# Performance work log

Measured on AMD Instinct MI355X. Metric: run time of the kernel, lower is better.

Reference implementation:

```python
import jax, jax.numpy as jnp
import numpy as np

N = 50000
E = 800000
IN, HID, OUT, HEADS = 128, 64, 64, 3
NEG_SLOPE = 0.2
BN_EPS = 1e-5


def setup_inputs() -> dict:
    key = jax.random.key(0)
    ks = jax.random.split(key, 20)
    s = 0.05
    inp = {
        "x": jax.random.normal(ks[0], (N, IN), jnp.float32),
        "edge_index": jax.random.randint(ks[1], (2, E), 0, N, jnp.int32),
        # layer 0: in=128 -> heads=3, C=64 (concat -> 192)
        "Wl0": jax.random.normal(ks[2], (IN, HEADS * HID), jnp.float32) * s,
        "bl0": jnp.zeros((HEADS * HID,), jnp.float32),
        "Wr0": jax.random.normal(ks[3], (IN, HEADS * HID), jnp.float32) * s,
        "br0": jnp.zeros((HEADS * HID,), jnp.float32),
        "att0": jax.random.normal(ks[4], (HEADS, HID), jnp.float32) * s,
        "bias0": jnp.zeros((HEADS * HID,), jnp.float32),
        "gamma0": jnp.ones((HEADS * HID,), jnp.float32),
        "beta0": jnp.zeros((HEADS * HID,), jnp.float32),
        # layer 1: in=192 -> heads=1, C=64
        "Wl1": jax.random.normal(ks[5], (HEADS * HID, OUT), jnp.float32) * s,
        "bl1": jnp.zeros((OUT,), jnp.float32),
        "Wr1": jax.random.normal(ks[6], (HEADS * HID, OUT), jnp.float32) * s,
        "br1": jnp.zeros((OUT,), jnp.float32),
        "att1": jax.random.normal(ks[7], (1, OUT), jnp.float32) * s,
        "bias1": jnp.zeros((OUT,), jnp.float32),
        "gamma1": jnp.ones((OUT,), jnp.float32),
        "beta1": jnp.zeros((OUT,), jnp.float32),
    }
    return inp


def _gatv2_layer(x, Wl, bl, Wr, br, att, bias, src, dst, n):
    H, C = att.shape
    xl = (x @ Wl + bl).reshape(n, H, C)
    xr = (x @ Wr + br).reshape(n, H, C)
    e = jax.nn.leaky_relu(xl[src] + xr[dst], NEG_SLOPE)      # [E,H,C]
    logit = jnp.einsum("ehc,hc->eh", e, att)                 # [E,H]
    m = jax.lax.stop_gradient(jax.ops.segment_max(logit, dst, num_segments=n))
    p = jnp.exp(logit - m[dst])
    denom = jax.ops.segment_sum(p, dst, num_segments=n)
    alpha = p / denom[dst]                                   # per-dst softmax
    out = jax.ops.segment_sum(alpha[:, :, None] * xl[src], dst, num_segments=n)
    return out.reshape(n, H * C) + bias


def _bn(x, gamma, beta):
    mu = x.mean(0)
    var = x.var(0)
    return (x - mu) * jax.lax.rsqrt(var + BN_EPS) * gamma + beta


def reference(x, edge_index, Wl0, bl0, Wr0, br0, att0, bias0, gamma0, beta0,
              Wl1, bl1, Wr1, br1, att1, bias1, gamma1, beta1):
    n = x.shape[0]
    loops = jnp.arange(n, dtype=edge_index.dtype)
    src = jnp.concatenate([edge_index[0], loops])  # PyG add_self_loops=True
    dst = jnp.concatenate([edge_index[1], loops])
    h = _gatv2_layer(x, Wl0, bl0, Wr0, br0, att0, bias0, src, dst, n)
    h = _bn(jax.nn.relu(h), gamma0, beta0)
    h = _gatv2_layer(h, Wl1, bl1, Wr1, br1, att1, bias1, src, dst, n)
    h = _bn(jax.nn.relu(h), gamma1, beta1)
    return h
```

## Files before the change

kernel.cpp:

```cpp
#include <hip/hip_runtime.h>
#include <hip/hip_bf16.h>

#define LRELU_SLOPE 0.2f
#define BN_EPS 1e-5f

typedef __attribute__((ext_vector_type(8))) short short8v;
typedef __attribute__((ext_vector_type(4))) float float4v;

static __device__ __forceinline__ unsigned short f2bf(float f) {
    __hip_bfloat16 b = __float2bfloat16(f);
    return *reinterpret_cast<unsigned short*>(&b);
}
static __device__ __forceinline__ float bf2f(unsigned short u) {
    return __uint_as_float(((unsigned)u) << 16);
}
static __device__ __forceinline__ void unpack2(unsigned int u, float& f0, float& f1) {
    f0 = __uint_as_float(u << 16);
    f1 = __uint_as_float(u & 0xffff0000u);
}

__global__ void convert_w2_kernel(const float* __restrict__ Wl0, const float* __restrict__ Wr0,
                                  const float* __restrict__ Wl1, const float* __restrict__ Wr1,
                                  unsigned short* __restrict__ Wt0, unsigned short* __restrict__ Wt1) {
    int idx = blockIdx.x * blockDim.x + threadIdx.x;
    if (idx < 384 * 128) {
        int c = idx >> 7, k = idx & 127;
        float v = (c < 192) ? Wl0[(size_t)k * 192 + c] : Wr0[(size_t)k * 192 + (c - 192)];
        Wt0[idx] = f2bf(v);
    } else if (idx < 384 * 128 + 128 * 192) {
        int i2 = idx - 384 * 128;
        int c = i2 / 192, k = i2 % 192;
        float v = (c < 64) ? Wl1[(size_t)k * 64 + c] : Wr1[(size_t)k * 64 + (c - 64)];
        Wt1[i2] = f2bf(v);
    }
}

__global__ void count_dst_kernel(const int* __restrict__ dst, int* __restrict__ counts, int E) {
    int e = blockIdx.x * blockDim.x + threadIdx.x;
    if (e < E) atomicAdd(&counts[dst[e]], 1);
}

__global__ void scanA_kernel(const int* __restrict__ counts, int* __restrict__ offs,
                             int* __restrict__ blkSum, int n) {
    __shared__ int wsum[4];
    const int lane = threadIdx.x & 63;
    const int wv = threadIdx.x >> 6;
    int i0 = blockIdx.x * 1024 + (int)threadIdx.x * 4;
    int v0 = (i0 + 0 < n) ? counts[i0 + 0] : 0;
    int v1 = (i0 + 1 < n) ? counts[i0 + 1] : 0;
    int v2 = (i0 + 2 < n) ? counts[i0 + 2] : 0;
    int v3 = (i0 + 3 < n) ? counts[i0 + 3] : 0;
    int s4 = v0 + v1 + v2 + v3;
    int s = s4;
    #pragma unroll
    for (int off = 1; off < 64; off <<= 1) {
        int t = __shfl_up(s, off, 64);
        if (lane >= off) s += t;
    }
    if (lane == 63) wsum[wv] = s;
    __syncthreads();
    int wpre = 0;
    for (int w = 0; w < wv; ++w) wpre += wsum[w];
    int excl = wpre + s - s4;
    if (i0 + 0 < n) offs[i0 + 0] = excl;
    excl += v0;
    if (i0 + 1 < n) offs[i0 + 1] = excl;
    excl += v1;
    if (i0 + 2 < n) offs[i0 + 2] = excl;
    excl += v2;
    if (i0 + 3 < n) offs[i0 + 3] = excl;
    if (threadIdx.x == 255) blkSum[blockIdx.x] = wpre + s;
}

__global__ void scanC_kernel(int* __restrict__ offs, const int* __restrict__ blkSum, int n, int E) {
    __shared__ int baseSh;
    const int b = blockIdx.x;
    if (threadIdx.x < 64) {
        int acc = 0;
        for (int i = threadIdx.x; i < b; i += 64) acc += blkSum[i];
        #pragma unroll
        for (int off = 1; off < 64; off <<= 1) acc += __shfl_xor(acc, off, 64);
        if (threadIdx.x == 0) baseSh = acc;
    }
    __syncthreads();
    const int base = baseSh;
    int i = b * 1024 + (int)threadIdx.x * 4;
    if (i + 3 < n) {
        int4 v = *reinterpret_cast<int4*>(&offs[i]);
        v.x += base; v.y += base; v.z += base; v.w += base;
        *reinterpret_cast<int4*>(&offs[i]) = v;
    } else {
        #pragma unroll
        for (int k = 0; k < 4; ++k)
            if (i + k < n) offs[i + k] += base;
    }
    if (b == 0 && threadIdx.x == 0) offs[n] = E;
}

__global__ void scatter_kernel(const int* __restrict__ src, const int* __restrict__ dst,
                               const int* __restrict__ offs, int* __restrict__ cursor,
                               int* __restrict__ esrc, int E) {
    int e = blockIdx.x * blockDim.x + threadIdx.x;
    if (e < E) {
        int d = dst[e];
        int pos = offs[d] + atomicAdd(&cursor[d], 1);
        esrc[pos] = src[e];
    }
}

template <int K, int NCH, bool BN>
__global__ __launch_bounds__(256) void mfma_dual_gemm(
    const float* __restrict__ X,
    const unsigned short* __restrict__ Wt,
    const float* __restrict__ bl, const float* __restrict__ br,
    const float* __restrict__ stats, const float* __restrict__ gamma,
    const float* __restrict__ beta, float invN,
    unsigned short* __restrict__ out, int N) {
    constexpr int ST = 2 * NCH;
    constexpr int LDA = 40;
    const int rowBase = blockIdx.x * 128;
    const int colBase = blockIdx.y * 128;

    __shared__ unsigned short XS[128 * LDA];
    __shared__ unsigned short WS[128 * LDA];
    __shared__ float ssA[K], ssB[K];

    const int tid = threadIdx.x;
    const int lane = tid & 63;
    const int wv = tid >> 6;
    const int lrow = lane & 15;
    const int lk = lane >> 4;

    if (BN) {
        for (int c = tid; c < K; c += 256) {
            float mu = stats[c] * invN;
            float var = stats[K + c] * invN - mu * mu;
            float sc = gamma[c] * rsqrtf(var + BN_EPS);
            ssA[c] = sc;
            ssB[c] = beta[c] - mu * sc;
        }
        __syncthreads();
    }

    float4v acc[2][8];
    #pragma unroll
    for (int i = 0; i < 2; ++i)
        #pragma unroll
        for (int j = 0; j < 8; ++j) acc[i][j] = (float4v){0.f, 0.f, 0.f, 0.f};

    for (int k0 = 0; k0 < K; k0 += 32) {
        {
            int r = tid >> 3;
            int kq = (tid & 7) * 4;
            float4 sc0, sc1;
            if (BN) {
                sc0 = *reinterpret_cast<const float4*>(&ssA[k0 + kq]);
                sc1 = *reinterpret_cast<const float4*>(&ssB[k0 + kq]);
            }
            #pragma unroll
            for (int i = 0; i < 4; ++i) {
                int row = r + 32 * i;
                int gr = rowBase + row;
                float4 v = make_float4(0.f, 0.f, 0.f, 0.f);
                if (gr < N) v = *reinterpret_cast<const float4*>(&X[(size_t)gr * K + k0 + kq]);
                if (BN) {
                    v.x = v.x * sc0.x + sc1.x;
                    v.y = v.y * sc0.y + sc1.y;
                    v.z = v.z * sc0.z + sc1.z;
                    v.w = v.w * sc0.w + sc1.w;
                }
                ushort4 u;
                u.x = f2bf(v.x); u.y = f2bf(v.y); u.z = f2bf(v.z); u.w = f2bf(v.w);
                *reinterpret_cast<ushort4*>(&XS[row * LDA + kq]) = u;
            }
        }
        {
            int c = tid >> 2;
            int kq8 = (tid & 3) * 8;
            #pragma unroll
            for (int i = 0; i < 2; ++i) {
                int col = c + 64 * i;
                uint4 w = *reinterpret_cast<const uint4*>(&Wt[(size_t)(colBase + col) * K + k0 + kq8]);
                *reinterpret_cast<uint4*>(&WS[col * LDA + kq8]) = w;
            }
        }
        __syncthreads();
        short8v aF[2], bF[8];
        #pragma unroll
        for (int rb = 0; rb < 2; ++rb)
            aF[rb] = *reinterpret_cast<const short8v*>(&XS[(wv * 32 + rb * 16 + lrow) * LDA + lk * 8]);
        #pragma unroll
        for (int cb = 0; cb < 8; ++cb)
            bF[cb] = *reinterpret_cast<const short8v*>(&WS[(cb * 16 + lrow) * LDA + lk * 8]);
        #pragma unroll
        for (int rb = 0; rb < 2; ++rb)
            #pragma unroll
            for (int cb = 0; cb < 8; ++cb)
                acc[rb][cb] = __builtin_amdgcn_mfma_f32_16x16x32_bf16(aF[rb], bF[cb], acc[rb][cb], 0, 0, 0);
        __syncthreads();
    }
    #pragma unroll
    for (int cb = 0; cb < 8; ++cb) {
        int cg = colBase + cb * 16 + lrow;
        float bv = (cg < NCH) ? bl[cg] : br[cg - NCH];
        #pragma unroll
        for (int rb = 0; rb < 2; ++rb) {
            #pragma unroll
            for (int r = 0; r < 4; ++r) {
                int row = rowBase + wv * 32 + rb * 16 + lk * 4 + r;
                if (row < N) out[(size_t)row * ST + cg] = f2bf(acc[rb][cb][r] + bv);
            }
        }
    }
}

template <int H>
__global__ __launch_bounds__(256) void gat_agg_kernel(
    const unsigned short* __restrict__ proj,
    const int* __restrict__ offs, const int* __restrict__ esrc,
    const float* __restrict__ att, const float* __restrict__ bias,
    float* __restrict__ outh, int N) {
    constexpr int C = 64;
    constexpr int HC = H * C;
    constexpr int ST = 2 * HC;
    const int lane = threadIdx.x & 63;
    const int node = blockIdx.x * 4 + (threadIdx.x >> 6);
    if (node >= N) return;
    const int j = lane >> 4;
    const int cg = (lane & 15) * 4;

    float4 xr4[H], att4[H], acc4[H];
    float den[H];
    #pragma unroll
    for (int h = 0; h < H; ++h) {
        ushort4 u = *reinterpret_cast<const ushort4*>(&proj[(size_t)node * ST + HC + h * C + cg]);
        xr4[h] = make_float4(bf2f(u.x), bf2f(u.y), bf2f(u.z), bf2f(u.w));
        att4[h] = *reinterpret_cast<const float4*>(&att[h * C + cg]);
        acc4[h] = make_float4(0.f, 0.f, 0.f, 0.f);
        den[h] = 0.f;
    }

    const int beg = offs[node];
    const int total = offs[node + 1] - beg + 1;
    int vc0 = (j < total) ? j : (total - 1);
    int srcN = (vc0 == 0) ? node : esrc[beg + vc0 - 1];
    ushort4 uN[H];
    #pragma unroll
    for (int h = 0; h < H; ++h)
        uN[h] = *reinterpret_cast<const ushort4*>(&proj[(size_t)srcN * ST + h * C + cg]);

    for (int t = 0; t < total; t += 4) {
        ushort4 uC[H];
        #pragma unroll
        for (int h = 0; h < H; ++h) uC[h] = uN[h];
        const int v = t + j;
        const float w = (v < total) ? 1.f : 0.f;
        const int v2 = v + 4;
        if (v2 < total) {
            int s2 = esrc[beg + v2 - 1];
            #pragma unroll
            for (int h = 0; h < H; ++h)
                uN[h] = *reinterpret_cast<const ushort4*>(&proj[(size_t)s2 * ST + h * C + cg]);
        }
        float4 xl4[H];
        float s[H];
        #pragma unroll
        for (int h = 0; h < H; ++h)
            xl4[h] = make_float4(bf2f(uC[h].x), bf2f(uC[h].y), bf2f(uC[h].z), bf2f(uC[h].w));
        #pragma unroll
        for (int h = 0; h < H; ++h) {
            float a0 = xl4[h].x + xr4[h].x;
            float a1 = xl4[h].y + xr4[h].y;
            float a2 = xl4[h].z + xr4[h].z;
            float a3 = xl4[h].w + xr4[h].w;
            a0 = (a0 > 0.f) ? a0 : LRELU_SLOPE * a0;
            a1 = (a1 > 0.f) ? a1 : LRELU_SLOPE * a1;
            a2 = (a2 > 0.f) ? a2 : LRELU_SLOPE * a2;
            a3 = (a3 > 0.f) ? a3 : LRELU_SLOPE * a3;
            s[h] = a0 * att4[h].x + a1 * att4[h].y + a2 * att4[h].z + a3 * att4[h].w;
        }
        #pragma unroll
        for (int off = 1; off <= 8; off <<= 1)
            #pragma unroll
            for (int h = 0; h < H; ++h) s[h] += __shfl_xor(s[h], off, 64);
        #pragma unroll
        for (int h = 0; h < H; ++h) {
            float p = w * __expf(s[h]);
            den[h] += p;
            acc4[h].x += p * xl4[h].x;
            acc4[h].y += p * xl4[h].y;
            acc4[h].z += p * xl4[h].z;
            acc4[h].w += p * xl4[h].w;
        }
    }

    #pragma unroll
    for (int off = 16; off <= 32; off <<= 1) {
        #pragma unroll
        for (int h = 0; h < H; ++h) {
            acc4[h].x += __shfl_xor(acc4[h].x, off, 64);
            acc4[h].y += __shfl_xor(acc4[h].y, off, 64);
            acc4[h].z += __shfl_xor(acc4[h].z, off, 64);
            acc4[h].w += __shfl_xor(acc4[h].w, off, 64);
            den[h]    += __shfl_xor(den[h],    off, 64);
        }
    }

    if (j == 0) {
        #pragma unroll
        for (int h = 0; h < H; ++h) {
            float4 b4 = *reinterpret_cast<const float4*>(&bias[h * C + cg]);
            float inv = 1.f / den[h];
            float4 o;
            o.x = acc4[h].x * inv + b4.x;
            o.y = acc4[h].y * inv + b4.y;
            o.z = acc4[h].z * inv + b4.z;
            o.w = acc4[h].w * inv + b4.w;
            o.x = (o.x > 0.f) ? o.x : 0.f;
            o.y = (o.y > 0.f) ? o.y : 0.f;
            o.z = (o.z > 0.f) ? o.z : 0.f;
            o.w = (o.w > 0.f) ? o.w : 0.f;
            *reinterpret_cast<float4*>(&outh[(size_t)node * HC + h * C + cg]) = o;
        }
    }
}

__global__ __launch_bounds__(256) void gat_agg1_kernel(
    const unsigned short* __restrict__ proj,
    const int* __restrict__ offs, const int* __restrict__ esrc,
    const float* __restrict__ att, const float* __restrict__ bias,
    float* __restrict__ outh, int N) {
    const int lane = threadIdx.x & 63;
    const int node = blockIdx.x * 4 + (threadIdx.x >> 6);
    if (node >= N) return;
    const int j = lane >> 3;
    const int cg = (lane & 7) * 8;

    float xr[8], at[8], acc[8];
    float den = 0.f;
    {
        uint4 u = *reinterpret_cast<const uint4*>(&proj[(size_t)node * 128 + 64 + cg]);
        unpack2(u.x, xr[0], xr[1]); unpack2(u.y, xr[2], xr[3]);
        unpack2(u.z, xr[4], xr[5]); unpack2(u.w, xr[6], xr[7]);
        float4 a0 = *reinterpret_cast<const float4*>(&att[cg]);
        float4 a1 = *reinterpret_cast<const float4*>(&att[cg + 4]);
        at[0] = a0.x; at[1] = a0.y; at[2] = a0.z; at[3] = a0.w;
        at[4] = a1.x; at[5] = a1.y; at[6] = a1.z; at[7] = a1.w;
        #pragma unroll
        for (int c = 0; c < 8; ++c) acc[c] = 0.f;
    }

    const int beg = offs[node];
    const int total = offs[node + 1] - beg + 1;
    int vc0 = (j < total) ? j : (total - 1);
    int srcN = (vc0 == 0) ? node : esrc[beg + vc0 - 1];
    uint4 uN = *reinterpret_cast<const uint4*>(&proj[(size_t)srcN * 128 + cg]);

    for (int t = 0; t < total; t += 8) {
        uint4 uC = uN;
        const int v = t + j;
        const float w = (v < total) ? 1.f : 0.f;
        const int v2 = v + 8;
        if (v2 < total) {
            int s2 = esrc[beg + v2 - 1];
            uN = *reinterpret_cast<const uint4*>(&proj[(size_t)s2 * 128 + cg]);
        }
        float xl[8];
        unpack2(uC.x, xl[0], xl[1]); unpack2(uC.y, xl[2], xl[3]);
        unpack2(uC.z, xl[4], xl[5]); unpack2(uC.w, xl[6], xl[7]);
        float s = 0.f;
        #pragma unroll
        for (int c = 0; c < 8; ++c) {
            float a = xl[c] + xr[c];
            a = (a > 0.f) ? a : LRELU_SLOPE * a;
            s += a * at[c];
        }
        #pragma unroll
        for (int off = 1; off <= 4; off <<= 1) s += __shfl_xor(s, off, 64);
        float p = w * __expf(s);
        den += p;
        #pragma unroll
        for (int c = 0; c < 8; ++c) acc[c] += p * xl[c];
    }

    #pragma unroll
    for (int off = 8; off <= 32; off <<= 1) {
        den += __shfl_xor(den, off, 64);
        #pragma unroll
        for (int c = 0; c < 8; ++c) acc[c] += __shfl_xor(acc[c], off, 64);
    }

    if (j == 0) {
        float inv = 1.f / den;
        float4 b0 = *reinterpret_cast<const float4*>(&bias[cg]);
        float4 b1 = *reinterpret_cast<const float4*>(&bias[cg + 4]);
        float4 o0, o1;
        o0.x = acc[0] * inv + b0.x; o0.y = acc[1] * inv + b0.y;
        o0.z = acc[2] * inv + b0.z; o0.w = acc[3] * inv + b0.w;
        o1.x = acc[4] * inv + b1.x; o1.y = acc[5] * inv + b1.y;
        o1.z = acc[6] * inv + b1.z; o1.w = acc[7] * inv + b1.w;
        o0.x = (o0.x > 0.f) ? o0.x : 0.f; o0.y = (o0.y > 0.f) ? o0.y : 0.f;
        o0.z = (o0.z > 0.f) ? o0.z : 0.f; o0.w = (o0.w > 0.f) ? o0.w : 0.f;
        o1.x = (o1.x > 0.f) ? o1.x : 0.f; o1.y = (o1.y > 0.f) ? o1.y : 0.f;
        o1.z = (o1.z > 0.f) ? o1.z : 0.f; o1.w = (o1.w > 0.f) ? o1.w : 0.f;
        *reinterpret_cast<float4*>(&outh[(size_t)node * 64 + cg]) = o0;
        *reinterpret_cast<float4*>(&outh[(size_t)node * 64 + cg + 4]) = o1;
    }
}

template <int CH>
__global__ void bn_stats_kernel(const float* __restrict__ h, float* __restrict__ stats, int N) {
    const int c = threadIdx.x;
    float s = 0.f, q = 0.f;
    for (int r = blockIdx.x; r < N; r += gridDim.x) {
        float v = h[(size_t)r * CH + c];
        s += v;
        q += v * v;
    }
    atomicAdd(&stats[c], s);
    atomicAdd(&stats[CH + c], q);
}

__global__ void bn_finapply64_kernel(float* __restrict__ h, const float* __restrict__ stats,
                                     const float* __restrict__ gamma, const float* __restrict__ beta,
                                     float invN, size_t total4) {
    size_t i = (size_t)blockIdx.x * blockDim.x + threadIdx.x;
    if (i >= total4) return;
    size_t e = i * 4;
    int c = (int)(e & 63);
    float4 v = *reinterpret_cast<float4*>(&h[e]);
    #pragma unroll
    for (int k = 0; k < 4; ++k) {
        float mu = stats[c + k] * invN;
        float var = stats[64 + c + k] * invN - mu * mu;
        float sc = gamma[c + k] * rsqrtf(var + BN_EPS);
        (&v.x)[k] = ((&v.x)[k] - mu) * sc + beta[c + k];
    }
    *reinterpret_cast<float4*>(&h[e]) = v;
}

extern "C" void kernel_launch(void* const* d_in, const int* in_sizes, int n_in,
                              void* d_out, int out_size, void* d_ws, size_t ws_size,
                              hipStream_t stream) {
    const float* x     = (const float*)d_in[0];
    const int*   eidx  = (const int*)d_in[1];
    const float* Wl0   = (const float*)d_in[2];
    const float* bl0   = (const float*)d_in[3];
    const float* Wr0   = (const float*)d_in[4];
    const float* br0   = (const float*)d_in[5];
    const float* att0  = (const float*)d_in[6];
    const float* bias0 = (const float*)d_in[7];
    const float* g0    = (const float*)d_in[8];
    const float* be0   = (const float*)d_in[9];
    const float* Wl1   = (const float*)d_in[10];
    const float* bl1   = (const float*)d_in[11];
    const float* Wr1   = (const float*)d_in[12];
    const float* br1   = (const float*)d_in[13];
    const float* att1  = (const float*)d_in[14];
    const float* bias1 = (const float*)d_in[15];
    const float* g1    = (const float*)d_in[16];
    const float* be1   = (const float*)d_in[17];

    const int N = in_sizes[0] / 128;
    const int E = in_sizes[1] / 2;
    const int* srcIdx = eidx;
    const int* dstIdx = eidx + E;
    const int nChunks = (N + 1023) >> 10;
    const float invN = 1.f / (float)N;

    char* base = (char*)d_ws;
    auto alloc = [&](size_t bytes) {
        char* p = base;
        base += (bytes + 255) & ~(size_t)255;
        return p;
    };
    unsigned short* proj = (unsigned short*)alloc((size_t)N * 384 * 2);
    float* h0    = (float*)alloc((size_t)N * 192 * 4);
    int*   offs  = (int*)alloc((size_t)(N + 1) * 4);
    int*   esrc  = (int*)alloc((size_t)E * 4);
    int*   blkSum= (int*)alloc((size_t)nChunks * 4);
    unsigned short* Wt0 = (unsigned short*)alloc((size_t)384 * 128 * 2);
    unsigned short* Wt1 = (unsigned short*)alloc((size_t)128 * 192 * 2);
    char* zeroBeg = base;
    int*   counts = (int*)alloc((size_t)N * 4);
    int*   cursor = (int*)alloc((size_t)N * 4);
    float* stats0 = (float*)alloc(384 * 4);
    float* stats1 = (float*)alloc(128 * 4);
    size_t zeroBytes = (size_t)(base - zeroBeg);

    hipMemsetAsync(zeroBeg, 0, zeroBytes, stream);
    convert_w2_kernel<<<(384 * 128 + 128 * 192 + 255) / 256, 256, 0, stream>>>(Wl0, Wr0, Wl1, Wr1, Wt0, Wt1);

    count_dst_kernel<<<(E + 255) / 256, 256, 0, stream>>>(dstIdx, counts, E);
    scanA_kernel<<<nChunks, 256, 0, stream>>>(counts, offs, blkSum, N);
    scanC_kernel<<<nChunks, 256, 0, stream>>>(offs, blkSum, N, E);
    scatter_kernel<<<(E + 255) / 256, 256, 0, stream>>>(srcIdx, dstIdx, offs, cursor, esrc, E);

    {
        dim3 grid((N + 127) / 128, 3);
        mfma_dual_gemm<128, 192, false><<<grid, 256, 0, stream>>>(
            x, Wt0, bl0, br0, nullptr, nullptr, nullptr, 0.f, proj, N);
    }
    gat_agg_kernel<3><<<(N + 3) / 4, 256, 0, stream>>>(proj, offs, esrc, att0, bias0, h0, N);
    bn_stats_kernel<192><<<256, 192, 0, stream>>>(h0, stats0, N);

    {
        dim3 grid((N + 127) / 128, 1);
        mfma_dual_gemm<192, 64, true><<<grid, 256, 0, stream>>>(
            h0, Wt1, bl1, br1, stats0, g0, be0, invN, proj, N);
    }
    float* out = (float*)d_out;
    gat_agg1_kernel<<<(N + 3) / 4, 256, 0, stream>>>(proj, offs, esrc, att1, bias1, out, N);
    bn_stats_kernel<64><<<256, 64, 0, stream>>>(out, stats1, N);
    {
        size_t tot4 = (size_t)N * 16;
        bn_finapply64_kernel<<<(unsigned)((tot4 + 255) / 256), 256, 0, stream>>>(out, stats1, g1, be1, invN, tot4);
    }
}
```

Measured before the change: 378.3 us.

## Fuse BN statistics into GAT aggregation with persistent blocks and deeper prefetch

The separate bn_stats kernels are removed. Each aggregation kernel now accumulates per-channel sum and sum-of-squares in LDS atomics and flushes them to global memory once per block. The kernels become grid-stride persistent with at most 1536 blocks, and the neighbor gather prefetch is deepened from one iteration ahead to two. This avoids re-reading h0 and the output for statistics, at the cost of LDS atomic contention and fewer resident blocks.

```diff
diff --git a/kernel.cpp b/kernel.cpp
--- a/kernel.cpp
+++ b/kernel.cpp
@@ -17,6 +17,9 @@
 static __device__ __forceinline__ void unpack2(unsigned int u, float& f0, float& f1) {
     f0 = __uint_as_float(u << 16);
     f1 = __uint_as_float(u & 0xffff0000u);
+}
+static __device__ __forceinline__ float lrelu(float x) {
+    return fmaxf(x, LRELU_SLOPE * x);
 }
 
 __global__ void convert_w2_kernel(const float* __restrict__ Wl0, const float* __restrict__ Wr0,
@@ -214,211 +217,227 @@
     }
 }
 
-template <int H>
-__global__ __launch_bounds__(256) void gat_agg_kernel(
+__global__ __launch_bounds__(256) void gat_agg3_bn_kernel(
     const unsigned short* __restrict__ proj,
     const int* __restrict__ offs, const int* __restrict__ esrc,
     const float* __restrict__ att, const float* __restrict__ bias,
-    float* __restrict__ outh, int N) {
-    constexpr int C = 64;
-    constexpr int HC = H * C;
-    constexpr int ST = 2 * HC;
-    const int lane = threadIdx.x & 63;
-    const int node = blockIdx.x * 4 + (threadIdx.x >> 6);
-    if (node >= N) return;
+    float* __restrict__ outh, float* __restrict__ stats,
+    int N, int nGroups) {
+    constexpr int H = 3, C = 64, HC = 192, ST = 384;
+    __shared__ float ldsStats[2 * HC];
+    const int tid = threadIdx.x;
+    const int lane = tid & 63;
+    const int wv = tid >> 6;
     const int j = lane >> 4;
     const int cg = (lane & 15) * 4;
 
-    float4 xr4[H], att4[H], acc4[H];
-    float den[H];
+    for (int i = tid; i < 2 * HC; i += 256) ldsStats[i] = 0.f;
+    __syncthreads();
+
+    float4 att4[H];
     #pragma unroll
-    for (int h = 0; h < H; ++h) {
-        ushort4 u = *reinterpret_cast<const ushort4*>(&proj[(size_t)node * ST + HC + h * C + cg]);
-        xr4[h] = make_float4(bf2f(u.x), bf2f(u.y), bf2f(u.z), bf2f(u.w));
-        att4[h] = *reinterpret_cast<const float4*>(&att[h * C + cg]);
-        acc4[h] = make_float4(0.f, 0.f, 0.f, 0.f);
-        den[h] = 0.f;
-    }
-
-    const int beg = offs[node];
-    const int total = offs[node + 1] - beg + 1;
-    int vc0 = (j < total) ? j : (total - 1);
-    int srcN = (vc0 == 0) ? node : esrc[beg + vc0 - 1];
-    ushort4 uN[H];
-    #pragma unroll
-    for (int h = 0; h < H; ++h)
-        uN[h] = *reinterpret_cast<const ushort4*>(&proj[(size_t)srcN * ST + h * C + cg]);
-
-    for (int t = 0; t < total; t += 4) {
-        ushort4 uC[H];
-        #pragma unroll
-        for (int h = 0; h < H; ++h) uC[h] = uN[h];
-        const int v = t + j;
-        const float w = (v < total) ? 1.f : 0.f;
-        const int v2 = v + 4;
-        if (v2 < total) {
-            int s2 = esrc[beg + v2 - 1];
+    for (int h = 0; h < H; ++h) att4[h] = *reinterpret_cast<const float4*>(&att[h * C + cg]);
+
+    for (int g = blockIdx.x; g < nGroups; g += gridDim.x) {
+        const int node = g * 4 + wv;
+        if (node >= N) continue;
+        float4 xr4[H], acc4[H];
+        float den[H];
+        #pragma unroll
+        for (int h = 0; h < H; ++h) {
+            ushort4 u = *reinterpret_cast<const ushort4*>(&proj[(size_t)node * ST + HC + h * C + cg]);
+            xr4[h] = make_float4(bf2f(u.x), bf2f(u.y), bf2f(u.z), bf2f(u.w));
+            acc4[h] = make_float4(0.f, 0.f, 0.f, 0.f);
+            den[h] = 0.f;
+        }
+        const int beg = offs[node];
+        const int total = offs[node + 1] - beg + 1;
+        ushort4 u0[H], u1[H];
+        {
+            int vc = (j < total) ? j : (total - 1);
+            int s0 = (vc == 0) ? node : esrc[beg + vc - 1];
             #pragma unroll
             for (int h = 0; h < H; ++h)
-                uN[h] = *reinterpret_cast<const ushort4*>(&proj[(size_t)s2 * ST + h * C + cg]);
-        }
-        float4 xl4[H];
-        float s[H];
-        #pragma unroll
-        for (int h = 0; h < H; ++h)
-            xl4[h] = make_float4(bf2f(uC[h].x), bf2f(uC[h].y), bf2f(uC[h].z), bf2f(uC[h].w));
-        #pragma unroll
-        for (int h = 0; h < H; ++h) {
-            float a0 = xl4[h].x + xr4[h].x;
-            float a1 = xl4[h].y + xr4[h].y;
-            float a2 = xl4[h].z + xr4[h].z;
-            float a3 = xl4[h].w + xr4[h].w;
-            a0 = (a0 > 0.f) ? a0 : LRELU_SLOPE * a0;
-            a1 = (a1 > 0.f) ? a1 : LRELU_SLOPE * a1;
-            a2 = (a2 > 0.f) ? a2 : LRELU_SLOPE * a2;
-            a3 = (a3 > 0.f) ? a3 : LRELU_SLOPE * a3;
-            s[h] = a0 * att4[h].x + a1 * att4[h].y + a2 * att4[h].z + a3 * att4[h].w;
-        }
-        #pragma unroll
-        for (int off = 1; off <= 8; off <<= 1)
-            #pragma unroll
-            for (int h = 0; h < H; ++h) s[h] += __shfl_xor(s[h], off, 64);
-        #pragma unroll
-        for (int h = 0; h < H; ++h) {
-            float p = w * __expf(s[h]);
-            den[h] += p;
-            acc4[h].x += p * xl4[h].x;
-            acc4[h].y += p * xl4[h].y;
-            acc4[h].z += p * xl4[h].z;
-            acc4[h].w += p * xl4[h].w;
-        }
-    }
-
-    #pragma unroll
-    for (int off = 16; off <= 32; off <<= 1) {
-        #pragma unroll
-        for (int h = 0; h < H; ++h) {
-            acc4[h].x += __shfl_xor(acc4[h].x, off, 64);
-            acc4[h].y += __shfl_xor(acc4[h].y, off, 64);
-            acc4[h].z += __shfl_xor(acc4[h].z, off, 64);
-            acc4[h].w += __shfl_xor(acc4[h].w, off, 64);
-            den[h]    += __shfl_xor(den[h],    off, 64);
-        }
-    }
-
-    if (j == 0) {
-        #pragma unroll
-        for (int h = 0; h < H; ++h) {
-            float4 b4 = *reinterpret_cast<const float4*>(&bias[h * C + cg]);
-            float inv = 1.f / den[h];
-            float4 o;
-            o.x = acc4[h].x * inv + b4.x;
-            o.y = acc4[h].y * inv + b4.y;
-            o.z = acc4[h].z * inv + b4.z;
-            o.w = acc4[h].w * inv + b4.w;
-            o.x = (o.x > 0.f) ? o.x : 0.f;
-            o.y = (o.y > 0.f) ? o.y : 0.f;
-            o.z = (o.z > 0.f) ? o.z : 0.f;
-            o.w = (o.w > 0.f) ? o.w : 0.f;
-            *reinterpret_cast<float4*>(&outh[(size_t)node * HC + h * C + cg]) = o;
-        }
-    }
-}
-
-__global__ __launch_bounds__(256) void gat_agg1_kernel(
+                u0[h] = *reinterpret_cast<const ushort4*>(&proj[(size_t)s0 * ST + h * C + cg]);
+            int v1i = j + 4;
+            int vc1 = (v1i < total) ? v1i : (total - 1);
+            int s1 = (vc1 == 0) ? node : esrc[beg + vc1 - 1];
+            #pragma unroll
+            for (int h = 0; h < H; ++h)
+                u1[h] = *reinterpret_cast<const ushort4*>(&proj[(size_t)s1 * ST + h * C + cg]);
+        }
+        for (int t = 0; t < total; t += 4) {
+            float4 xl4[H];
+            #pragma unroll
+            for (int h = 0; h < H; ++h) {
+                xl4[h] = make_float4(bf2f(u0[h].x), bf2f(u0[h].y), bf2f(u0[h].z), bf2f(u0[h].w));
+                u0[h] = u1[h];
+            }
+            const int v2 = t + 8 + j;
+            if (v2 < total) {
+                int s2 = esrc[beg + v2 - 1];
+                #pragma unroll
+                for (int h = 0; h < H; ++h)
+                    u1[h] = *reinterpret_cast<const ushort4*>(&proj[(size_t)s2 * ST + h * C + cg]);
+            }
+            float s[H];
+            #pragma unroll
+            for (int h = 0; h < H; ++h) {
+                float a0 = lrelu(xl4[h].x + xr4[h].x);
+                float a1 = lrelu(xl4[h].y + xr4[h].y);
+                float a2 = lrelu(xl4[h].z + xr4[h].z);
+                float a3 = lrelu(xl4[h].w + xr4[h].w);
+                s[h] = a0 * att4[h].x + a1 * att4[h].y + a2 * att4[h].z + a3 * att4[h].w;
+            }
+            #pragma unroll
+            for (int off = 1; off <= 8; off <<= 1)
+                #pragma unroll
+                for (int h = 0; h < H; ++h) s[h] += __shfl_xor(s[h], off, 64);
+            const float w = (t + j < total) ? 1.f : 0.f;
+            #pragma unroll
+            for (int h = 0; h < H; ++h) {
+                float p = w * __expf(s[h]);
+                den[h] += p;
+                acc4[h].x += p * xl4[h].x;
+                acc4[h].y += p * xl4[h].y;
+                acc4[h].z += p * xl4[h].z;
+                acc4[h].w += p * xl4[h].w;
+            }
+        }
+        #pragma unroll
+        for (int off = 16; off <= 32; off <<= 1) {
+            #pragma unroll
+            for (int h = 0; h < H; ++h) {
+                acc4[h].x += __shfl_xor(acc4[h].x, off, 64);
+                acc4[h].y += __shfl_xor(acc4[h].y, off, 64);
+                acc4[h].z += __shfl_xor(acc4[h].z, off, 64);
+                acc4[h].w += __shfl_xor(acc4[h].w, off, 64);
+                den[h]    += __shfl_xor(den[h],    off, 64);
+            }
+        }
+        if (j == 0) {
+            #pragma unroll
+            for (int h = 0; h < H; ++h) {
+                float4 b4 = *reinterpret_cast<const float4*>(&bias[h * C + cg]);
+                float inv = 1.f / den[h];
+                float4 o;
+                o.x = fmaxf(acc4[h].x * inv + b4.x, 0.f);
+                o.y = fmaxf(acc4[h].y * inv + b4.y, 0.f);
+                o.z = fmaxf(acc4[h].z * inv + b4.z, 0.f);
+                o.w = fmaxf(acc4[h].w * inv + b4.w, 0.f);
+                *reinterpret_cast<float4*>(&outh[(size_t)node * HC + h * C + cg]) = o;
+                atomicAdd(&ldsStats[h * C + cg + 0], o.x);
+                atomicAdd(&ldsStats[h * C + cg + 1], o.y);
+                atomicAdd(&ldsStats[h * C + cg + 2], o.z);
+                atomicAdd(&ldsStats[h * C + cg + 3], o.w);
+                atomicAdd(&ldsStats[HC + h * C + cg + 0], o.x * o.x);
+                atomicAdd(&ldsStats[HC + h * C + cg + 1], o.y * o.y);
+                atomicAdd(&ldsStats[HC + h * C + cg + 2], o.z * o.z);
+                atomicAdd(&ldsStats[HC + h * C + cg + 3], o.w * o.w);
+            }
+        }
+    }
+    __syncthreads();
+    for (int i = tid; i < 2 * HC; i += 256) atomicAdd(&stats[i], ldsStats[i]);
+}
+
+__global__ __launch_bounds__(256) void gat_agg1_bn_kernel(
     const unsigned short* __restrict__ proj,
     const int* __restrict__ offs, const int* __restrict__ esrc,
     const float* __restrict__ att, const float* __restrict__ bias,
-    float* __restrict__ outh, int N) {
-    const int lane = threadIdx.x & 63;
-    const int node = blockIdx.x * 4 + (threadIdx.x >> 6);
-    if (node >= N) return;
+    float* __restrict__ outh, float* __restrict__ stats,
+    int N, int nGroups) {
+    __shared__ float ldsStats[128];
+    const int tid = threadIdx.x;
+    const int lane = tid & 63;
+    const int wv = tid >> 6;
     const int j = lane >> 3;
     const int cg = (lane & 7) * 8;
 
-    float xr[8], at[8], acc[8];
-    float den = 0.f;
+    for (int i = tid; i < 128; i += 256) ldsStats[i] = 0.f;
+    __syncthreads();
+
+    float at[8];
     {
-        uint4 u = *reinterpret_cast<const uint4*>(&proj[(size_t)node * 128 + 64 + cg]);
-        unpack2(u.x, xr[0], xr[1]); unpack2(u.y, xr[2], xr[3]);
-        unpack2(u.z, xr[4], xr[5]); unpack2(u.w, xr[6], xr[7]);
         float4 a0 = *reinterpret_cast<const float4*>(&att[cg]);
         float4 a1 = *reinterpret_cast<const float4*>(&att[cg + 4]);
         at[0] = a0.x; at[1] = a0.y; at[2] = a0.z; at[3] = a0.w;
         at[4] = a1.x; at[5] = a1.y; at[6] = a1.z; at[7] = a1.w;
-        #pragma unroll
-        for (int c = 0; c < 8; ++c) acc[c] = 0.f;
-    }
-
-    const int beg = offs[node];
-    const int total = offs[node + 1] - beg + 1;
-    int vc0 = (j < total) ? j : (total - 1);
-    int srcN = (vc0 == 0) ? node : esrc[beg + vc0 - 1];
-    uint4 uN = *reinterpret_cast<const uint4*>(&proj[(size_t)srcN * 128 + cg]);
-
-    for (int t = 0; t < total; t += 8) {
-        uint4 uC = uN;
-        const int v = t + j;
-        const float w = (v < total) ? 1.f : 0.f;
-        const int v2 = v + 8;
-        if (v2 < total) {
-            int s2 = esrc[beg + v2 - 1];
-            uN = *reinterpret_cast<const uint4*>(&proj[(size_t)s2 * 128 + cg]);
-        }
-        float xl[8];
-        unpack2(uC.x, xl[0], xl[1]); unpack2(uC.y, xl[2], xl[3]);
-        unpack2(uC.z, xl[4], xl[5]); unpack2(uC.w, xl[6], xl[7]);
-        float s = 0.f;
-        #pragma unroll
-        for (int c = 0; c < 8; ++c) {
-            float a = xl[c] + xr[c];
-            a = (a > 0.f) ? a : LRELU_SLOPE * a;
-            s += a * at[c];
-        }
-        #pragma unroll
-        for (int off = 1; off <= 4; off <<= 1) s += __shfl_xor(s, off, 64);
-        float p = w * __expf(s);
-        den += p;
-        #pragma unroll
-        for (int c = 0; c < 8; ++c) acc[c] += p * xl[c];
-    }
-
-    #pragma unroll
-    for (int off = 8; off <= 32; off <<= 1) {
-        den += __shfl_xor(den, off, 64);
-        #pragma unroll
-        for (int c = 0; c < 8; ++c) acc[c] += __shfl_xor(acc[c], off, 64);
-    }
-
-    if (j == 0) {
-        float inv = 1.f / den;
-        float4 b0 = *reinterpret_cast<const float4*>(&bias[cg]);
-        float4 b1 = *reinterpret_cast<const float4*>(&bias[cg + 4]);
-        float4 o0, o1;
-        o0.x = acc[0] * inv + b0.x; o0.y = acc[1] * inv + b0.y;
-        o0.z = acc[2] * inv + b0.z; o0.w = acc[3] * inv + b0.w;
-        o1.x = acc[4] * inv + b1.x; o1.y = acc[5] * inv + b1.y;
-        o1.z = acc[6] * inv + b1.z; o1.w = acc[7] * inv + b1.w;
-        o0.x = (o0.x > 0.f) ? o0.x : 0.f; o0.y = (o0.y > 0.f) ? o0.y : 0.f;
-        o0.z = (o0.z > 0.f) ? o0.z : 0.f; o0.w = (o0.w > 0.f) ? o0.w : 0.f;
-        o1.x = (o1.x > 0.f) ? o1.x : 0.f; o1.y = (o1.y > 0.f) ? o1.y : 0.f;
-        o1.z = (o1.z > 0.f) ? o1.z : 0.f; o1.w = (o1.w > 0.f) ? o1.w : 0.f;
-        *reinterpret_cast<float4*>(&outh[(size_t)node * 64 + cg]) = o0;
-        *reinterpret_cast<float4*>(&outh[(size_t)node * 64 + cg + 4]) = o1;
-    }
-}
-
-template <int CH>
-__global__ void bn_stats_kernel(const float* __restrict__ h, float* __restrict__ stats, int N) {
-    const int c = threadIdx.x;
-    float s = 0.f, q = 0.f;
-    for (int r = blockIdx.x; r < N; r += gridDim.x) {
-        float v = h[(size_t)r * CH + c];
-        s += v;
-        q += v * v;
-    }
-    atomicAdd(&stats[c], s);
-    atomicAdd(&stats[CH + c], q);
+    }
+
+    for (int g = blockIdx.x; g < nGroups; g += gridDim.x) {
+        const int node = g * 4 + wv;
+        if (node >= N) continue;
+        float xr[8], acc[8];
+        float den = 0.f;
+        {
+            uint4 u = *reinterpret_cast<const uint4*>(&proj[(size_t)node * 128 + 64 + cg]);
+            unpack2(u.x, xr[0], xr[1]); unpack2(u.y, xr[2], xr[3]);
+            unpack2(u.z, xr[4], xr[5]); unpack2(u.w, xr[6], xr[7]);
+            #pragma unroll
+            for (int c = 0; c < 8; ++c) acc[c] = 0.f;
+        }
+        const int beg = offs[node];
+        const int total = offs[node + 1] - beg + 1;
+        uint4 u0, u1;
+        {
+            int vc = (j < total) ? j : (total - 1);
+            int s0 = (vc == 0) ? node : esrc[beg + vc - 1];
+            u0 = *reinterpret_cast<const uint4*>(&proj[(size_t)s0 * 128 + cg]);
+            int v1i = j + 8;
+            int vc1 = (v1i < total) ? v1i : (total - 1);
+            int s1 = (vc1 == 0) ? node : esrc[beg + vc1 - 1];
+            u1 = *reinterpret_cast<const uint4*>(&proj[(size_t)s1 * 128 + cg]);
+        }
+        for (int t = 0; t < total; t += 8) {
+            float xl[8];
+            unpack2(u0.x, xl[0], xl[1]); unpack2(u0.y, xl[2], xl[3]);
+            unpack2(u0.z, xl[4], xl[5]); unpack2(u0.w, xl[6], xl[7]);
+            u0 = u1;
+            const int v2 = t + 16 + j;
+            if (v2 < total) {
+                int s2 = esrc[beg + v2 - 1];
+                u1 = *reinterpret_cast<const uint4*>(&proj[(size_t)s2 * 128 + cg]);
+            }
+            float s = 0.f;
+            #pragma unroll
+            for (int c = 0; c < 8; ++c) s += lrelu(xl[c] + xr[c]) * at[c];
+            #pragma unroll
+            for (int off = 1; off <= 4; off <<= 1) s += __shfl_xor(s, off, 64);
+            const float w = (t + j < total) ? 1.f : 0.f;
+            float p = w * __expf(s);
+            den += p;
+            #pragma unroll
+            for (int c = 0; c < 8; ++c) acc[c] += p * xl[c];
+        }
+        #pragma unroll
+        for (int off = 8; off <= 32; off <<= 1) {
+            den += __shfl_xor(den, off, 64);
+            #pragma unroll
+            for (int c = 0; c < 8; ++c) acc[c] += __shfl_xor(acc[c], off, 64);
+        }
+        if (j == 0) {
+            float inv = 1.f / den;
+            float4 b0 = *reinterpret_cast<const float4*>(&bias[cg]);
+            float4 b1 = *reinterpret_cast<const float4*>(&bias[cg + 4]);
+            float o[8];
+            o[0] = fmaxf(acc[0] * inv + b0.x, 0.f); o[1] = fmaxf(acc[1] * inv + b0.y, 0.f);
+            o[2] = fmaxf(acc[2] * inv + b0.z, 0.f); o[3] = fmaxf(acc[3] * inv + b0.w, 0.f);
+            o[4] = fmaxf(acc[4] * inv + b1.x, 0.f); o[5] = fmaxf(acc[5] * inv + b1.y, 0.f);
+            o[6] = fmaxf(acc[6] * inv + b1.z, 0.f); o[7] = fmaxf(acc[7] * inv + b1.w, 0.f);
+            float4 w0 = make_float4(o[0], o[1], o[2], o[3]);
+            float4 w1 = make_float4(o[4], o[5], o[6], o[7]);
+            *reinterpret_cast<float4*>(&outh[(size_t)node * 64 + cg]) = w0;
+            *reinterpret_cast<float4*>(&outh[(size_t)node * 64 + cg + 4]) = w1;
+            #pragma unroll
+            for (int c = 0; c < 8; ++c) {
+                atomicAdd(&ldsStats[cg + c], o[c]);
+                atomicAdd(&ldsStats[64 + cg + c], o[c] * o[c]);
+            }
+        }
+    }
+    __syncthreads();
+    for (int i = tid; i < 128; i += 256) atomicAdd(&stats[i], ldsStats[i]);
 }
 
 __global__ void bn_finapply64_kernel(float* __restrict__ h, const float* __restrict__ stats,
@@ -466,6 +485,7 @@
     const int* srcIdx = eidx;
     const int* dstIdx = eidx + E;
     const int nChunks = (N + 1023) >> 10;
+    const int nGroups = (N + 3) / 4;
     const float invN = 1.f / (float)N;
 
     char* base = (char*)d_ws;
@@ -501,8 +521,10 @@
         mfma_dual_gemm<128, 192, false><<<grid, 256, 0, stream>>>(
             x, Wt0, bl0, br0, nullptr, nullptr, nullptr, 0.f, proj, N);
     }
-    gat_agg_kernel<3><<<(N + 3) / 4, 256, 0, stream>>>(proj, offs, esrc, att0, bias0, h0, N);
-    bn_stats_kernel<192><<<256, 192, 0, stream>>>(h0, stats0, N);
+    {
+        int blocks = nGroups < 1536 ? nGroups : 1536;
+        gat_agg3_bn_kernel<<<blocks, 256, 0, stream>>>(proj, offs, esrc, att0, bias0, h0, stats0, N, nGroups);
+    }
 
     {
         dim3 grid((N + 127) / 128, 1);
@@ -510,8 +532,10 @@
             h0, Wt1, bl1, br1, stats0, g0, be0, invN, proj, N);
     }
     float* out = (float*)d_out;
-    gat_agg1_kernel<<<(N + 3) / 4, 256, 0, stream>>>(proj, offs, esrc, att1, bias1, out, N);
-    bn_stats_kernel<64><<<256, 64, 0, stream>>>(out, stats1, N);
+    {
+        int blocks = nGroups < 1536 ? nGroups : 1536;
+        gat_agg1_bn_kernel<<<blocks, 256, 0, stream>>>(proj, offs, esrc, att1, bias1, out, stats1, N, nGroups);
+    }
     {
         size_t tot4 = (size_t)N * 16;
         bn_finapply64_kernel<<<(unsigned)((tot4 + 255) / 256), 256, 0, stream>>>(out, stats1, g1, be1, invN, tot4);
```

New measurement: 391.0 us. 3.4% more time.

## Split projections into per-head planar buffers and aggregate one head per block

Applied to the files above, without the earlier changes.

The GEMM epilogue now writes xl and xr into separate head-major planar arrays of [N,64] bf16 instead of one interleaved [N,384] row. Both GAT layers use a single head-generic aggregation kernel that launches a grid dimension per head, so each gathered source row is a contiguous 128-byte segment. The gather is also prefetched two iterations ahead. This is meant to shrink the per-node gather footprint so the per-head working set fits better in cache. In exchange, the edge list and softmax work are repeated once per head, and the GEMM stores become strided per column.

```diff
diff --git a/kernel.cpp b/kernel.cpp
--- a/kernel.cpp
+++ b/kernel.cpp
@@ -11,12 +11,12 @@
     __hip_bfloat16 b = __float2bfloat16(f);
     return *reinterpret_cast<unsigned short*>(&b);
 }
-static __device__ __forceinline__ float bf2f(unsigned short u) {
-    return __uint_as_float(((unsigned)u) << 16);
-}
 static __device__ __forceinline__ void unpack2(unsigned int u, float& f0, float& f1) {
     f0 = __uint_as_float(u << 16);
     f1 = __uint_as_float(u & 0xffff0000u);
+}
+static __device__ __forceinline__ float lrelu(float x) {
+    return fmaxf(x, LRELU_SLOPE * x);
 }
 
 __global__ void convert_w2_kernel(const float* __restrict__ Wl0, const float* __restrict__ Wr0,
@@ -115,8 +115,7 @@
     const float* __restrict__ bl, const float* __restrict__ br,
     const float* __restrict__ stats, const float* __restrict__ gamma,
     const float* __restrict__ beta, float invN,
-    unsigned short* __restrict__ out, int N) {
-    constexpr int ST = 2 * NCH;
+    unsigned short* __restrict__ xlB, unsigned short* __restrict__ xrB, int N) {
     constexpr int LDA = 40;
     const int rowBase = blockIdx.x * 128;
     const int colBase = blockIdx.y * 128;
@@ -201,135 +200,36 @@
     }
     #pragma unroll
     for (int cb = 0; cb < 8; ++cb) {
-        int cg = colBase + cb * 16 + lrow;
-        float bv = (cg < NCH) ? bl[cg] : br[cg - NCH];
+        int cgG = colBase + cb * 16 + lrow;
+        bool isR = cgG >= NCH;
+        int cc = isR ? cgG - NCH : cgG;
+        int hh = cc >> 6;
+        int ch = cc & 63;
+        float bv = isR ? br[cc] : bl[cc];
+        unsigned short* dstB = (isR ? xrB : xlB) + (size_t)hh * N * 64 + ch;
         #pragma unroll
         for (int rb = 0; rb < 2; ++rb) {
             #pragma unroll
             for (int r = 0; r < 4; ++r) {
                 int row = rowBase + wv * 32 + rb * 16 + lk * 4 + r;
-                if (row < N) out[(size_t)row * ST + cg] = f2bf(acc[rb][cb][r] + bv);
+                if (row < N) dstB[(size_t)row * 64] = f2bf(acc[rb][cb][r] + bv);
             }
         }
     }
 }
 
 template <int H>
-__global__ __launch_bounds__(256) void gat_agg_kernel(
-    const unsigned short* __restrict__ proj,
+__global__ __launch_bounds__(256) void gat_agg_head_kernel(
+    const unsigned short* __restrict__ xlB,
+    const unsigned short* __restrict__ xrB,
     const int* __restrict__ offs, const int* __restrict__ esrc,
-    const float* __restrict__ att, const float* __restrict__ bias,
-    float* __restrict__ outh, int N) {
-    constexpr int C = 64;
-    constexpr int HC = H * C;
-    constexpr int ST = 2 * HC;
-    const int lane = threadIdx.x & 63;
-    const int node = blockIdx.x * 4 + (threadIdx.x >> 6);
-    if (node >= N) return;
-    const int j = lane >> 4;
-    const int cg = (lane & 15) * 4;
-
-    float4 xr4[H], att4[H], acc4[H];
-    float den[H];
-    #pragma unroll
-    for (int h = 0; h < H; ++h) {
-        ushort4 u = *reinterpret_cast<const ushort4*>(&proj[(size_t)node * ST + HC + h * C + cg]);
-        xr4[h] = make_float4(bf2f(u.x), bf2f(u.y), bf2f(u.z), bf2f(u.w));
-        att4[h] = *reinterpret_cast<const float4*>(&att[h * C + cg]);
-        acc4[h] = make_float4(0.f, 0.f, 0.f, 0.f);
-        den[h] = 0.f;
-    }
-
-    const int beg = offs[node];
-    const int total = offs[node + 1] - beg + 1;
-    int vc0 = (j < total) ? j : (total - 1);
-    int srcN = (vc0 == 0) ? node : esrc[beg + vc0 - 1];
-    ushort4 uN[H];
-    #pragma unroll
-    for (int h = 0; h < H; ++h)
-        uN[h] = *reinterpret_cast<const ushort4*>(&proj[(size_t)srcN * ST + h * C + cg]);
-
-    for (int t = 0; t < total; t += 4) {
-        ushort4 uC[H];
-        #pragma unroll
-        for (int h = 0; h < H; ++h) uC[h] = uN[h];
-        const int v = t + j;
-        const float w = (v < total) ? 1.f : 0.f;
-        const int v2 = v + 4;
-        if (v2 < total) {
-            int s2 = esrc[beg + v2 - 1];
-            #pragma unroll
-            for (int h = 0; h < H; ++h)
-                uN[h] = *reinterpret_cast<const ushort4*>(&proj[(size_t)s2 * ST + h * C + cg]);
-        }
-        float4 xl4[H];
-        float s[H];
-        #pragma unroll
-        for (int h = 0; h < H; ++h)
-            xl4[h] = make_float4(bf2f(uC[h].x), bf2f(uC[h].y), bf2f(uC[h].z), bf2f(uC[h].w));
-        #pragma unroll
-        for (int h = 0; h < H; ++h) {
-            float a0 = xl4[h].x + xr4[h].x;
-            float a1 = xl4[h].y + xr4[h].y;
-            float a2 = xl4[h].z + xr4[h].z;
-            float a3 = xl4[h].w + xr4[h].w;
-            a0 = (a0 > 0.f) ? a0 : LRELU_SLOPE * a0;
-            a1 = (a1 > 0.f) ? a1 : LRELU_SLOPE * a1;
-            a2 = (a2 > 0.f) ? a2 : LRELU_SLOPE * a2;
-            a3 = (a3 > 0.f) ? a3 : LRELU_SLOPE * a3;
-            s[h] = a0 * att4[h].x + a1 * att4[h].y + a2 * att4[h].z + a3 * att4[h].w;
-        }
-        #pragma unroll
-        for (int off = 1; off <= 8; off <<= 1)
-            #pragma unroll
-            for (int h = 0; h < H; ++h) s[h] += __shfl_xor(s[h], off, 64);
-        #pragma unroll
-        for (int h = 0; h < H; ++h) {
-            float p = w * __expf(s[h]);
-            den[h] += p;
-            acc4[h].x += p * xl4[h].x;
-            acc4[h].y += p * xl4[h].y;
-            acc4[h].z += p * xl4[h].z;
-            acc4[h].w += p * xl4[h].w;
-        }
-    }
-
-    #pragma unroll
-    for (int off = 16; off <= 32; off <<= 1) {
-        #pragma unroll
-        for (int h = 0; h < H; ++h) {
-            acc4[h].x += __shfl_xor(acc4[h].x, off, 64);
-            acc4[h].y += __shfl_xor(acc4[h].y, off, 64);
-            acc4[h].z += __shfl_xor(acc4[h].z, off, 64);
-            acc4[h].w += __shfl_xor(acc4[h].w, off, 64);
-            den[h]    += __shfl_xor(den[h],    off, 64);
-        }
-    }
-
-    if (j == 0) {
-        #pragma unroll
-        for (int h = 0; h < H; ++h) {
-            float4 b4 = *reinterpret_cast<const float4*>(&bias[h * C + cg]);
-            float inv = 1.f / den[h];
-            float4 o;
-            o.x = acc4[h].x * inv + b4.x;
-            o.y = acc4[h].y * inv + b4.y;
-            o.z = acc4[h].z * inv + b4.z;
-            o.w = acc4[h].w * inv + b4.w;
-            o.x = (o.x > 0.f) ? o.x : 0.f;
-            o.y = (o.y > 0.f) ? o.y : 0.f;
-            o.z = (o.z > 0.f) ? o.z : 0.f;
-            o.w = (o.w > 0.f) ? o.w : 0.f;
-            *reinterpret_cast<float4*>(&outh[(size_t)node * HC + h * C + cg]) = o;
-        }
-    }
-}
-
-__global__ __launch_bounds__(256) void gat_agg1_kernel(
-    const unsigned short* __restrict__ proj,
-    const int* __restrict__ offs, const int* __restrict__ esrc,
-    const float* __restrict__ att, const float* __restrict__ bias,
-    float* __restrict__ outh, int N) {
+    const float* __restrict__ att,
+    const float* __restrict__ bias,
+    float* __restrict__ outh,
+    int N) {
+    const int h = blockIdx.y;
+    const unsigned short* xl_ = xlB + (size_t)h * N * 64;
+    const unsigned short* xr_ = xrB + (size_t)h * N * 64;
     const int lane = threadIdx.x & 63;
     const int node = blockIdx.x * 4 + (threadIdx.x >> 6);
     if (node >= N) return;
@@ -339,11 +239,11 @@
     float xr[8], at[8], acc[8];
     float den = 0.f;
     {
-        uint4 u = *reinterpret_cast<const uint4*>(&proj[(size_t)node * 128 + 64 + cg]);
+        uint4 u = *reinterpret_cast<const uint4*>(&xr_[(size_t)node * 64 + cg]);
         unpack2(u.x, xr[0], xr[1]); unpack2(u.y, xr[2], xr[3]);
         unpack2(u.z, xr[4], xr[5]); unpack2(u.w, xr[6], xr[7]);
-        float4 a0 = *reinterpret_cast<const float4*>(&att[cg]);
-        float4 a1 = *reinterpret_cast<const float4*>(&att[cg + 4]);
+        float4 a0 = *reinterpret_cast<const float4*>(&att[h * 64 + cg]);
+        float4 a1 = *reinterpret_cast<const float4*>(&att[h * 64 + cg + 4]);
         at[0] = a0.x; at[1] = a0.y; at[2] = a0.z; at[3] = a0.w;
         at[4] = a1.x; at[5] = a1.y; at[6] = a1.z; at[7] = a1.w;
         #pragma unroll
@@ -352,35 +252,36 @@
 
     const int beg = offs[node];
     const int total = offs[node + 1] - beg + 1;
-    int vc0 = (j < total) ? j : (total - 1);
-    int srcN = (vc0 == 0) ? node : esrc[beg + vc0 - 1];
-    uint4 uN = *reinterpret_cast<const uint4*>(&proj[(size_t)srcN * 128 + cg]);
-
+    uint4 u0, u1;
+    {
+        int vc = (j < total) ? j : (total - 1);
+        int s0 = (vc == 0) ? node : esrc[beg + vc - 1];
+        u0 = *reinterpret_cast<const uint4*>(&xl_[(size_t)s0 * 64 + cg]);
+        int v1i = j + 8;
+        int vc1 = (v1i < total) ? v1i : (total - 1);
+        int s1 = (vc1 == 0) ? node : esrc[beg + vc1 - 1];
+        u1 = *reinterpret_cast<const uint4*>(&xl_[(size_t)s1 * 64 + cg]);
+    }
     for (int t = 0; t < total; t += 8) {
-        uint4 uC = uN;
-        const int v = t + j;
-        const float w = (v < total) ? 1.f : 0.f;
-        const int v2 = v + 8;
+        float xlv[8];
+        unpack2(u0.x, xlv[0], xlv[1]); unpack2(u0.y, xlv[2], xlv[3]);
+        unpack2(u0.z, xlv[4], xlv[5]); unpack2(u0.w, xlv[6], xlv[7]);
+        u0 = u1;
+        const int v2 = t + 16 + j;
         if (v2 < total) {
             int s2 = esrc[beg + v2 - 1];
-            uN = *reinterpret_cast<const uint4*>(&proj[(size_t)s2 * 128 + cg]);
+            u1 = *reinterpret_cast<const uint4*>(&xl_[(size_t)s2 * 64 + cg]);
         }
-        float xl[8];
-        unpack2(uC.x, xl[0], xl[1]); unpack2(uC.y, xl[2], xl[3]);
-        unpack2(uC.z, xl[4], xl[5]); unpack2(uC.w, xl[6], xl[7]);
         float s = 0.f;
         #pragma unroll
-        for (int c = 0; c < 8; ++c) {
-            float a = xl[c] + xr[c];
-            a = (a > 0.f) ? a : LRELU_SLOPE * a;
-            s += a * at[c];
-        }
+        for (int c = 0; c < 8; ++c) s += lrelu(xlv[c] + xr[c]) * at[c];
         #pragma unroll
         for (int off = 1; off <= 4; off <<= 1) s += __shfl_xor(s, off, 64);
+        const float w = (t + j < total) ? 1.f : 0.f;
         float p = w * __expf(s);
         den += p;
         #pragma unroll
-        for (int c = 0; c < 8; ++c) acc[c] += p * xl[c];
+        for (int c = 0; c < 8; ++c) acc[c] += p * xlv[c];
     }
 
     #pragma unroll
@@ -392,19 +293,16 @@
 
     if (j == 0) {
         float inv = 1.f / den;
-        float4 b0 = *reinterpret_cast<const float4*>(&bias[cg]);
-        float4 b1 = *reinterpret_cast<const float4*>(&bias[cg + 4]);
+        float4 b0 = *reinterpret_cast<const float4*>(&bias[h * 64 + cg]);
+        float4 b1 = *reinterpret_cast<const float4*>(&bias[h * 64 + cg + 4]);
         float4 o0, o1;
-        o0.x = acc[0] * inv + b0.x; o0.y = acc[1] * inv + b0.y;
-        o0.z = acc[2] * inv + b0.z; o0.w = acc[3] * inv + b0.w;
-        o1.x = acc[4] * inv + b1.x; o1.y = acc[5] * inv + b1.y;
-        o1.z = acc[6] * inv + b1.z; o1.w = acc[7] * inv + b1.w;
-        o0.x = (o0.x > 0.f) ? o0.x : 0.f; o0.y = (o0.y > 0.f) ? o0.y : 0.f;
-        o0.z = (o0.z > 0.f) ? o0.z : 0.f; o0.w = (o0.w > 0.f) ? o0.w : 0.f;
-        o1.x = (o1.x > 0.f) ? o1.x : 0.f; o1.y = (o1.y > 0.f) ? o1.y : 0.f;
-        o1.z = (o1.z > 0.f) ? o1.z : 0.f; o1.w = (o1.w > 0.f) ? o1.w : 0.f;
-        *reinterpret_cast<float4*>(&outh[(size_t)node * 64 + cg]) = o0;
-        *reinterpret_cast<float4*>(&outh[(size_t)node * 64 + cg + 4]) = o1;
+        o0.x = fmaxf(acc[0] * inv + b0.x, 0.f); o0.y = fmaxf(acc[1] * inv + b0.y, 0.f);
+        o0.z = fmaxf(acc[2] * inv + b0.z, 0.f); o0.w = fmaxf(acc[3] * inv + b0.w, 0.f);
+        o1.x = fmaxf(acc[4] * inv + b1.x, 0.f); o1.y = fmaxf(acc[5] * inv + b1.y, 0.f);
+        o1.z = fmaxf(acc[6] * inv + b1.z, 0.f); o1.w = fmaxf(acc[7] * inv + b1.w, 0.f);
+        float* orow = &outh[(size_t)node * (H * 64) + h * 64 + cg];
+        *reinterpret_cast<float4*>(orow) = o0;
+        *reinterpret_cast<float4*>(orow + 4) = o1;
     }
 }
 
@@ -466,6 +364,7 @@
     const int* srcIdx = eidx;
     const int* dstIdx = eidx + E;
     const int nChunks = (N + 1023) >> 10;
+    const int nGroups = (N + 3) / 4;
     const float invN = 1.f / (float)N;
 
     char* base = (char*)d_ws;
@@ -474,7 +373,8 @@
         base += (bytes + 255) & ~(size_t)255;
         return p;
     };
-    unsigned short* proj = (unsigned short*)alloc((size_t)N * 384 * 2);
+    unsigned short* projL = (unsigned short*)alloc((size_t)3 * N * 64 * 2);
+    unsigned short* projR = (unsigned short*)alloc((size_t)3 * N * 64 * 2);
     float* h0    = (float*)alloc((size_t)N * 192 * 4);
     int*   offs  = (int*)alloc((size_t)(N + 1) * 4);
     int*   esrc  = (int*)alloc((size_t)E * 4);
@@ -499,18 +399,24 @@
     {
         dim3 grid((N + 127) / 128, 3);
         mfma_dual_gemm<128, 192, false><<<grid, 256, 0, stream>>>(
-            x, Wt0, bl0, br0, nullptr, nullptr, nullptr, 0.f, proj, N);
-    }
-    gat_agg_kernel<3><<<(N + 3) / 4, 256, 0, stream>>>(proj, offs, esrc, att0, bias0, h0, N);
+            x, Wt0, bl0, br0, nullptr, nullptr, nullptr, 0.f, projL, projR, N);
+    }
+    {
+        dim3 grid(nGroups, 3);
+        gat_agg_head_kernel<3><<<grid, 256, 0, stream>>>(projL, projR, offs, esrc, att0, bias0, h0, N);
+    }
     bn_stats_kernel<192><<<256, 192, 0, stream>>>(h0, stats0, N);
 
     {
         dim3 grid((N + 127) / 128, 1);
         mfma_dual_gemm<192, 64, true><<<grid, 256, 0, stream>>>(
-            h0, Wt1, bl1, br1, stats0, g0, be0, invN, proj, N);
+            h0, Wt1, bl1, br1, stats0, g0, be0, invN, projL, projR, N);
     }
     float* out = (float*)d_out;
-    gat_agg1_kernel<<<(N + 3) / 4, 256, 0, stream>>>(proj, offs, esrc, att1, bias1, out, N);
+    {
+        dim3 grid(nGroups, 1);
+        gat_agg_head_kernel<1><<<grid, 256, 0, stream>>>(projL, projR, offs, esrc, att1, bias1, out, N);
+    }
     bn_stats_kernel<64><<<256, 64, 0, stream>>>(out, stats1, N);
     {
         size_t tot4 = (size_t)N * 16;
```

Measured after the change: 382.1 us. No clear change (+1.0%).
